# Kernel optimization log

Measured on AMD Instinct MI355X. Metric: run time of the kernel, lower is better.

The kernel has to match this reference:

```python
import jax, jax.numpy as jnp
import numpy as np

H, F, K, R = 8, 64, 10, 256  # num_heads, in_features, num_sines, num_realizations
B, L = 4, 2048


def setup_inputs() -> dict:
    key = jax.random.key(0)
    k1, k2, k3, k4, k5, k6 = jax.random.split(key, 6)
    return {
        "queries": jax.random.normal(k1, (B, L, H, F), dtype=jnp.float32),
        "keys": jax.random.normal(k2, (B, L, H, F), dtype=jnp.float32),
        "z": jax.random.normal(k3, (B, H, F, 2 * K, R), dtype=jnp.float32),
        "freqs": jax.random.normal(k4, (H, F, K), dtype=jnp.float32),
        "offsets": jax.random.normal(k5, (H, F, K), dtype=jnp.float32),
        "gains": jax.random.normal(k6, (H, F, K), dtype=jnp.float32),
    }


def reference(queries, keys, z, freqs, offsets, gains):
    h, f_dim, k_sines = freqs.shape
    length = queries.shape[1]
    r = z.shape[-1]
    # split positional / non-positional features (rest is empty here: key_dim == in_features)
    q_pos, q_rest = queries[..., :f_dim], queries[..., f_dim:]
    k_pos, k_rest = keys[..., :f_dim], keys[..., f_dim:]

    idx = jnp.arange(length, dtype=queries.dtype)  # linspace(0, L-1, L)
    fr = jax.nn.sigmoid(freqs)[:, :, None, :] / 2.0          # [H, F, 1, K]
    base = 2.0 * jnp.pi * fr * idx[None, None, :, None]       # [H, F, L, K]
    ph_q = base + offsets[:, :, None, :]
    ph_k = base
    # stack(cos, sin) on last axis then flatten -> interleaved cos0,sin0,... : [H, F, L, 2K]
    omega_q = jnp.stack([jnp.cos(ph_q), jnp.sin(ph_q)], axis=-1).reshape(h, f_dim, length, 2 * k_sines)
    omega_k = jnp.stack([jnp.cos(ph_k), jnp.sin(ph_k)], axis=-1).reshape(h, f_dim, length, 2 * k_sines)

    g = jnp.tile(jax.nn.softplus(gains), (1, 1, 2))           # [H, F, 2K] (block-repeated, as in torch .repeat)
    zs = z * g[None, :, :, :, None] / np.sqrt(r * f_dim).astype(np.float32)  # [B, H, F, 2K, R]

    # fused double contraction over f (in_features) and s (2K sines); equals
    # (omega @ z) permuted then multiplied by queries and summed over in_features
    qhat = jnp.einsum('hfls,bhfsr,blhf->blhr', omega_q, zs, q_pos)  # [B, L, H, R]
    khat = jnp.einsum('hfls,bhfsr,blhf->blhr', omega_k, zs, k_pos)

    qhat = jnp.concatenate([qhat, q_rest], axis=-1)
    khat = jnp.concatenate([khat, k_rest], axis=-1)
    return qhat, khat
```

## Files before the change

### kernel.cpp

```cpp
#include <hip/hip_runtime.h>
#include <math.h>


#define NH 8
#define NF 64
#define NK 10
#define NR 256
#define NB 4
#define NL 2048
#define KTOT 1280
#define BM 128
#define BK 32
#define NCH (KTOT/BK)
#define NFRAG_B 16
#define WS_NEEDED ((size_t)NB*NH*NCH*NFRAG_B*1024)

typedef __attribute__((ext_vector_type(8))) short short8;
typedef __attribute__((ext_vector_type(4))) float f32x4;
typedef __attribute__((ext_vector_type(4))) unsigned int u32x4;

static __device__ __forceinline__ unsigned short f2b(float f) {
    unsigned x = __float_as_uint(f);
    return (unsigned short)((x + 0x7FFFu + ((x >> 16) & 1u)) >> 16);
}
static __device__ __forceinline__ unsigned int pk2(float a, float b) {
    return (unsigned int)f2b(a) | ((unsigned int)f2b(b) << 16);
}
static __device__ __forceinline__ void gload_lds16(const void* g, void* l) {
    __builtin_amdgcn_global_load_lds(
        (const __attribute__((address_space(1))) unsigned int*)g,
        (__attribute__((address_space(3))) unsigned int*)l, 16, 0, 0);
}

__global__ __launch_bounds__(256)
void spe_prep(const float* __restrict__ z, const float* __restrict__ gains,
              unsigned char* __restrict__ bpack)
{
    __shared__ float s_g[NF*NK];
    const int ch  = blockIdx.x;
    const int bh  = blockIdx.y;
    const int h   = bh & 7;
    const int tid = threadIdx.x;
    for (int i = tid; i < NF*NK; i += 256)
        s_g[i] = log1pf(expf(gains[h*NF*NK + i])) * 0.0078125f;
    __syncthreads();
    const float* zb = z + (size_t)bh * KTOT * NR;
    unsigned char* dst = bpack + ((size_t)(bh*NCH + ch) * NFRAG_B) * 1024;
    #pragma unroll
    for (int it = 0; it < 4; ++it) {
        const int s  = tid + 256*it;
        const int fi = s >> 6;
        const int l  = s & 63;
        const int r  = fi*16 + (l & 15);
        const int k0 = ch*BK + (l >> 4)*8;
        u32x4 wv;
        #pragma unroll
        for (int jp = 0; jp < 4; ++jp) {
            const int ka = k0 + 2*jp, kb = ka + 1;
            const int fa = (ka*3277) >> 16; int sa = ka - fa*20; if (sa >= NK) sa -= NK;
            const int fb = (kb*3277) >> 16; int sb = kb - fb*20; if (sb >= NK) sb -= NK;
            const float va = zb[(size_t)ka*NR + r] * s_g[fa*NK + sa];
            const float vb = zb[(size_t)kb*NR + r] * s_g[fb*NK + sb];
            wv[jp] = pk2(va, vb);
        }
        *(u32x4*)(dst + (size_t)s*16) = wv;
    }
}

#define OFF_B0  0
#define OFF_B1  16384
#define OFF_A   32768
#define OFF_POS 40960
#define OFF_FR  57344
#define OFF_OF  59904
#define SMEM_SZ 62464

__global__ __launch_bounds__(512, 4)
void spe_main(const float* __restrict__ queries, const float* __restrict__ keys,
              const float* __restrict__ freqs, const float* __restrict__ offsets,
              const unsigned char* __restrict__ bpack, float* __restrict__ out)
{
    __shared__ __attribute__((aligned(16))) unsigned char smem[SMEM_SZ];
    const int tid  = threadIdx.x;
    const int lane = tid & 63;
    const int w    = tid >> 6;
    const int l0   = blockIdx.x * BM;
    const int bh   = blockIdx.y;
    const int b = bh >> 3, h = bh & 7;
    const int isK  = blockIdx.z;

    float* ld_fr = (float*)(smem + OFF_FR);
    float* ld_of = (float*)(smem + OFF_OF);
    unsigned short* pos_t = (unsigned short*)(smem + OFF_POS);

    for (int i = tid; i < NF*NK; i += 512) {
        const float fv = freqs[h*NF*NK + i];
        ld_fr[i] = 0.5f / (1.0f + expf(-fv));
        ld_of[i] = isK ? 0.0f : offsets[h*NF*NK + i] * 0.15915494309189535f;
    }
    {
        const float* pos = isK ? keys : queries;
        const int r  = tid >> 2;
        const int f0 = (tid & 3) * 16;
        const float* src = pos + ((size_t)((b*NL + l0 + r)*NH + h))*NF + f0;
        #pragma unroll
        for (int j = 0; j < 4; ++j) {
            const float4 v = *(const float4*)(src + j*4);
            const int f = f0 + j*4;
            pos_t[(f+0)*BM + r] = f2b(v.x);
            pos_t[(f+1)*BM + r] = f2b(v.y);
            pos_t[(f+2)*BM + r] = f2b(v.z);
            pos_t[(f+3)*BM + r] = f2b(v.w);
        }
    }
    __syncthreads();

    const unsigned char* bp = bpack + (size_t)bh * ((size_t)NCH*NFRAG_B*1024);
    const int fi0 = w*2;
    gload_lds16(bp + (size_t)fi0*1024 + lane*16,       smem + OFF_B0 + (fi0  <<10));
    gload_lds16(bp + (size_t)(fi0+1)*1024 + lane*16,   smem + OFF_B0 + ((fi0+1)<<10));

    const int wm = w >> 2, wn = w & 3;
    f32x4 acc[4][4];
    #pragma unroll
    for (int mi = 0; mi < 4; ++mi)
        #pragma unroll
        for (int ni = 0; ni < 4; ++ni)
            acc[mi][ni] = (f32x4){0.f, 0.f, 0.f, 0.f};

    const int a_oct  = w >> 1;
    const int a_m    = ((w & 1) << 6) | lane;
    const float lf   = (float)(l0 + a_m);
    const int a_byte = (((w & 1)*4 + (lane >> 4)) << 10) + (a_oct << 8) + ((lane & 15) << 4);

    auto synthA = [&](int t) -> u32x4 {
        u32x4 wv;
        #pragma unroll
        for (int jp = 0; jp < 4; ++jp) {
            const int kk   = t*BK + a_oct*8 + 2*jp;
            const int f    = (kk*3277) >> 16;
            const int srem = kk - f*20;
            const int kidx = f*NK + (srem >> 1);
            const float x  = __builtin_amdgcn_fractf(ld_of[kidx] + ld_fr[kidx]*lf);
            const float c  = __builtin_amdgcn_cosf(x);
            const float sn = __builtin_amdgcn_sinf(x);
            const float p  = __uint_as_float(((unsigned)pos_t[f*BM + a_m]) << 16);
            wv[jp] = pk2(c*p, sn*p);
        }
        return wv;
    };

    u32x4 wv = synthA(0);

    for (int t = 0; t < NCH; ++t) {
        unsigned char* Bcur = smem + ((t & 1) ? OFF_B1 : OFF_B0);
        unsigned char* Bnxt = smem + ((t & 1) ? OFF_B0 : OFF_B1);

        asm volatile("s_waitcnt vmcnt(0)" ::: "memory");
        __builtin_amdgcn_sched_barrier(0);
        __builtin_amdgcn_s_barrier();

        if (t + 1 < NCH) {
            gload_lds16(bp + (size_t)((t+1)*NFRAG_B + fi0)*1024 + lane*16,
                        Bnxt + (fi0<<10));
            gload_lds16(bp + (size_t)((t+1)*NFRAG_B + fi0+1)*1024 + lane*16,
                        Bnxt + ((fi0+1)<<10));
        }

        *(u32x4*)(smem + OFF_A + a_byte) = wv;
        asm volatile("s_waitcnt lgkmcnt(0)" ::: "memory");
        __builtin_amdgcn_sched_barrier(0);
        __builtin_amdgcn_s_barrier();

        short8 bf[4];
        #pragma unroll
        for (int ni = 0; ni < 4; ++ni)
            bf[ni] = *(const short8*)(Bcur + ((wn*4 + ni) << 10) + (lane << 4));

        if (t + 1 < NCH) wv = synthA(t + 1);

        #pragma unroll
        for (int mi = 0; mi < 4; ++mi) {
            const short8 af = *(const short8*)(smem + OFF_A + ((wm*4 + mi) << 10) + (lane << 4));
            #pragma unroll
            for (int ni = 0; ni < 4; ++ni)
                acc[mi][ni] = __builtin_amdgcn_mfma_f32_16x16x32_bf16(af, bf[ni], acc[mi][ni], 0, 0, 0);
        }
    }

    const size_t qk_off = (size_t)isK * ((size_t)NB*NL*NH*NR);
    const int row_l = (lane >> 4) * 4;
    const int col_r = lane & 15;
    #pragma unroll
    for (int mi = 0; mi < 4; ++mi) {
        const int lg = l0 + wm*64 + mi*16 + row_l;
        #pragma unroll
        for (int ni = 0; ni < 4; ++ni) {
            const int rg = wn*64 + ni*16 + col_r;
            const f32x4 v = acc[mi][ni];
            #pragma unroll
            for (int q = 0; q < 4; ++q)
                out[qk_off + ((size_t)((b*NL + lg + q)*NH + h))*NR + rg] = v[q];
        }
    }
}

#define FOFF_B   0
#define FOFF_A   32768
#define FOFF_POS 49152
#define FOFF_FR  65536
#define FOFF_OFS 68096
#define FOFF_GS  70656
#define FSMEM_SZ 73216

__global__ __launch_bounds__(512, 4)
void spe_mfma_fb(const float* __restrict__ queries, const float* __restrict__ keys,
                 const float* __restrict__ z, const float* __restrict__ freqs,
                 const float* __restrict__ offsets, const float* __restrict__ gains,
                 float* __restrict__ out)
{
    __shared__ __attribute__((aligned(16))) unsigned char smem[FSMEM_SZ];
    const int tid = threadIdx.x, lane = tid & 63;
    const int l0 = blockIdx.x * BM, bh = blockIdx.y;
    const int b = bh >> 3, h = bh & 7, isK = blockIdx.z;
    float* ld_fr = (float*)(smem + FOFF_FR);
    float* ld_of = (float*)(smem + FOFF_OFS);
    float* ld_gs = (float*)(smem + FOFF_GS);
    unsigned short* pos_t = (unsigned short*)(smem + FOFF_POS);
    for (int i = tid; i < NF*NK; i += 512) {
        const float fv = freqs[h*NF*NK + i];
        ld_fr[i] = 0.5f / (1.0f + expf(-fv));
        ld_of[i] = isK ? 0.0f : offsets[h*NF*NK + i] * 0.15915494309189535f;
        ld_gs[i] = log1pf(expf(gains[h*NF*NK + i])) * 0.0078125f;
    }
    {
        const float* pos = isK ? keys : queries;
        #pragma unroll
        for (int i = 0; i < 4; ++i) {
            const int lrow = (tid >> 4) + 32*i;
            const int f0 = (tid & 15) * 4;
            const float4 v = *(const float4*)(pos + ((size_t)((b*NL + l0 + lrow)*NH + h))*NF + f0);
            pos_t[(f0+0)*BM + lrow] = f2b(v.x); pos_t[(f0+1)*BM + lrow] = f2b(v.y);
            pos_t[(f0+2)*BM + lrow] = f2b(v.z); pos_t[(f0+3)*BM + lrow] = f2b(v.w);
        }
    }
    __syncthreads();
    const int w = tid >> 6, wm = w >> 2, wn = w & 3;
    f32x4 acc[4][4];
    #pragma unroll
    for (int mi = 0; mi < 4; ++mi)
        #pragma unroll
        for (int ni = 0; ni < 4; ++ni) acc[mi][ni] = (f32x4){0.f,0.f,0.f,0.f};
    const float* zbh = z + (size_t)(b*NH + h) * ((size_t)KTOT*NR);
    for (int ch = 0; ch < KTOT/64; ++ch) {
        const int fs0 = ch * 64;
        #pragma unroll
        for (int i = 0; i < 4; ++i) {
            const int tau = tid + 512*i, r = tau & 255, krun = tau >> 8;
            const float* zp = zbh + (size_t)(fs0 + krun*8)*NR + r;
            u32x4 wv2;
            #pragma unroll
            for (int jp = 0; jp < 4; ++jp) {
                const int fs = fs0 + krun*8 + 2*jp;
                const int f = (fs*3277) >> 16; const int rem = fs - f*20;
                const int km = (rem >= NK) ? rem - NK : rem;
                const int kn = ((rem+1) >= NK && (rem+1) < 2*NK) ? rem+1-NK : rem+1;
                const float sc0 = ld_gs[f*NK + km], sc1 = ld_gs[f*NK + (kn < NK ? kn : kn-NK)];
                wv2[jp] = pk2(zp[(2*jp)*NR]*sc0, zp[(2*jp+1)*NR]*sc1);
            }
            *(u32x4*)(smem + FOFF_B + ((((krun>>2)*16) + (r>>4)) << 10)
                                    + ((((krun&3)*16) + (r&15)) << 4)) = wv2;
        }
        #pragma unroll
        for (int i = 0; i < 2; ++i) {
            const int tau = tid + 512*i, m = tau & 127, krun = tau >> 7;
            const float lff = (float)(l0 + m);
            u32x4 wv2;
            #pragma unroll
            for (int jp = 0; jp < 4; ++jp) {
                const int fs = fs0 + krun*8 + 2*jp;
                const int f = (fs*3277) >> 16; const int rem = fs - f*20;
                const int kidx = f*NK + (rem >> 1);
                const float x = __builtin_amdgcn_fractf(ld_of[kidx] + ld_fr[kidx]*lff);
                const float c = __builtin_amdgcn_cosf(x), sn = __builtin_amdgcn_sinf(x);
                const float p = __uint_as_float(((unsigned)pos_t[f*BM + m]) << 16);
                wv2[jp] = pk2(c*p, sn*p);
            }
            *(u32x4*)(smem + FOFF_A + ((((krun>>2)*8) + (m>>4)) << 10)
                                    + ((((krun&3)*16) + (m&15)) << 4)) = wv2;
        }
        __syncthreads();
        #pragma unroll
        for (int ks = 0; ks < 2; ++ks) {
            short8 bf[4];
            #pragma unroll
            for (int ni = 0; ni < 4; ++ni)
                bf[ni] = *(const short8*)(smem + FOFF_B + ((ks*16 + wn*4 + ni) << 10) + (lane << 4));
            #pragma unroll
            for (int mi = 0; mi < 4; ++mi) {
                const short8 af = *(const short8*)(smem + FOFF_A + ((ks*8 + wm*4 + mi) << 10) + (lane << 4));
                #pragma unroll
                for (int ni = 0; ni < 4; ++ni)
                    acc[mi][ni] = __builtin_amdgcn_mfma_f32_16x16x32_bf16(af, bf[ni], acc[mi][ni], 0, 0, 0);
            }
        }
        __syncthreads();
    }
    const size_t qk_off = (size_t)isK * ((size_t)NB*NL*NH*NR);
    const int row_l = (lane >> 4) * 4, col_r = lane & 15;
    #pragma unroll
    for (int mi = 0; mi < 4; ++mi) {
        const int lg = l0 + wm*64 + mi*16 + row_l;
        #pragma unroll
        for (int ni = 0; ni < 4; ++ni) {
            const int rg = wn*64 + ni*16 + col_r;
            const f32x4 v = acc[mi][ni];
            #pragma unroll
            for (int q = 0; q < 4; ++q)
                out[qk_off + ((size_t)((b*NL + lg + q)*NH + h))*NR + rg] = v[q];
        }
    }
}

extern "C" void kernel_launch(void* const* d_in, const int* in_sizes, int n_in,
                              void* d_out, int out_size, void* d_ws, size_t ws_size,
                              hipStream_t stream) {
    const float* queries = (const float*)d_in[0];
    const float* keys    = (const float*)d_in[1];
    const float* z       = (const float*)d_in[2];
    const float* freqs   = (const float*)d_in[3];
    const float* offsets = (const float*)d_in[4];
    const float* gains   = (const float*)d_in[5];
    float* out = (float*)d_out;

    if (ws_size >= WS_NEEDED) {
        unsigned char* bpack = (unsigned char*)d_ws;
        spe_prep<<<dim3(NCH, NB*NH), 256, 0, stream>>>(z, gains, bpack);
        spe_main<<<dim3(NL/BM, NB*NH, 2), 512, 0, stream>>>(queries, keys, freqs, offsets, bpack, out);
    } else {
        spe_mfma_fb<<<dim3(NL/BM, NB*NH, 2), 512, 0, stream>>>(queries, keys, z, freqs, offsets, gains, out);
    }
}
```

Measured before the change: 133.6 us.

## Fuse query and key tiles per block, sharing sin/cos via angle-addition

Each block now handles 64 positions for both queries and keys instead of 128 positions for one of them. The query phase is derived from the key phase with the angle-addition identity and precomputed cos/sin of the offsets, so only one sin/cos pair is evaluated per element. The change also switches to a hardware packed bf16 convert and XOR-swizzles the A-tile LDS layout to reduce bank conflicts. The grid stays the same size, and z tiles are loaded once for both outputs, at the cost of slightly more LDS and a few extra multiplies.

```diff
diff --git a/kernel.cpp b/kernel.cpp
--- a/kernel.cpp
+++ b/kernel.cpp
@@ -18,6 +18,7 @@
 typedef __attribute__((ext_vector_type(8))) short short8;
 typedef __attribute__((ext_vector_type(4))) float f32x4;
 typedef __attribute__((ext_vector_type(4))) unsigned int u32x4;
+typedef __attribute__((ext_vector_type(2))) unsigned int u32x2;
 
 static __device__ __forceinline__ unsigned short f2b(float f) {
     unsigned x = __float_as_uint(f);
@@ -25,6 +26,11 @@
 }
 static __device__ __forceinline__ unsigned int pk2(float a, float b) {
     return (unsigned int)f2b(a) | ((unsigned int)f2b(b) << 16);
+}
+static __device__ __forceinline__ unsigned int cvtpk(float lo, float hi) {
+    unsigned int r;
+    asm("v_cvt_pk_bf16_f32 %0, %1, %2" : "=v"(r) : "v"(lo), "v"(hi));
+    return r;
 }
 static __device__ __forceinline__ void gload_lds16(const void* g, void* l) {
     __builtin_amdgcn_global_load_lds(
@@ -72,8 +78,9 @@
 #define OFF_A   32768
 #define OFF_POS 40960
 #define OFF_FR  57344
-#define OFF_OF  59904
-#define SMEM_SZ 62464
+#define OFF_CO  59904
+#define OFF_SO  62464
+#define SMEM_SZ 65024
 
 __global__ __launch_bounds__(512, 4)
 void spe_main(const float* __restrict__ queries, const float* __restrict__ keys,
@@ -84,33 +91,38 @@
     const int tid  = threadIdx.x;
     const int lane = tid & 63;
     const int w    = tid >> 6;
-    const int l0   = blockIdx.x * BM;
+    const int l0   = blockIdx.x * 64;
     const int bh   = blockIdx.y;
     const int b = bh >> 3, h = bh & 7;
-    const int isK  = blockIdx.z;
 
     float* ld_fr = (float*)(smem + OFF_FR);
-    float* ld_of = (float*)(smem + OFF_OF);
+    float* ld_co = (float*)(smem + OFF_CO);
+    float* ld_so = (float*)(smem + OFF_SO);
     unsigned short* pos_t = (unsigned short*)(smem + OFF_POS);
 
     for (int i = tid; i < NF*NK; i += 512) {
         const float fv = freqs[h*NF*NK + i];
         ld_fr[i] = 0.5f / (1.0f + expf(-fv));
-        ld_of[i] = isK ? 0.0f : offsets[h*NF*NK + i] * 0.15915494309189535f;
+        const float xo = __builtin_amdgcn_fractf(offsets[h*NF*NK + i] * 0.15915494309189535f);
+        ld_co[i] = __builtin_amdgcn_cosf(xo);
+        ld_so[i] = __builtin_amdgcn_sinf(xo);
     }
     {
-        const float* pos = isK ? keys : queries;
         const int r  = tid >> 2;
         const int f0 = (tid & 3) * 16;
-        const float* src = pos + ((size_t)((b*NL + l0 + r)*NH + h))*NF + f0;
+        const int rl = r & 63;
+        const float* src = (r < 64)
+            ? queries + ((size_t)((b*NL + l0 + rl)*NH + h))*NF + f0
+            : keys    + ((size_t)((b*NL + l0 + rl)*NH + h))*NF + f0;
+        unsigned short* pdst = pos_t + ((r >> 6) << 12);
         #pragma unroll
         for (int j = 0; j < 4; ++j) {
             const float4 v = *(const float4*)(src + j*4);
             const int f = f0 + j*4;
-            pos_t[(f+0)*BM + r] = f2b(v.x);
-            pos_t[(f+1)*BM + r] = f2b(v.y);
-            pos_t[(f+2)*BM + r] = f2b(v.z);
-            pos_t[(f+3)*BM + r] = f2b(v.w);
+            pdst[(f+0)*64 + rl] = f2b(v.x);
+            pdst[(f+1)*64 + rl] = f2b(v.y);
+            pdst[(f+2)*64 + rl] = f2b(v.z);
+            pdst[(f+3)*64 + rl] = f2b(v.w);
         }
     }
     __syncthreads();
@@ -128,29 +140,38 @@
         for (int ni = 0; ni < 4; ++ni)
             acc[mi][ni] = (f32x4){0.f, 0.f, 0.f, 0.f};
 
-    const int a_oct  = w >> 1;
-    const int a_m    = ((w & 1) << 6) | lane;
-    const float lf   = (float)(l0 + a_m);
-    const int a_byte = (((w & 1)*4 + (lane >> 4)) << 10) + (a_oct << 8) + ((lane & 15) << 4);
-
-    auto synthA = [&](int t) -> u32x4 {
-        u32x4 wv;
-        #pragma unroll
-        for (int jp = 0; jp < 4; ++jp) {
-            const int kk   = t*BK + a_oct*8 + 2*jp;
+    const int rq   = tid & 63;
+    const int oct  = (tid >> 6) & 3;
+    const int half = tid >> 8;
+    const float lf = (float)(l0 + rq);
+    const unsigned short* posq = pos_t;
+    const unsigned short* posk = pos_t + 4096;
+    const int a_log_q = ((rq >> 4) << 10) + ((oct*16 + (rq & 15)) << 4) + (half << 3);
+    const int aw_q = a_log_q ^ (((rq >> 4) & 3) << 5);
+    const int aw_k = (a_log_q + 4096) ^ (((rq >> 4) & 3) << 5);
+
+    auto synthA = [&](int t, u32x2& q01, u32x2& k01) {
+        #pragma unroll
+        for (int p = 0; p < 2; ++p) {
+            const int kk   = t*BK + oct*8 + (half*2 + p)*2;
             const int f    = (kk*3277) >> 16;
             const int srem = kk - f*20;
             const int kidx = f*NK + (srem >> 1);
-            const float x  = __builtin_amdgcn_fractf(ld_of[kidx] + ld_fr[kidx]*lf);
-            const float c  = __builtin_amdgcn_cosf(x);
-            const float sn = __builtin_amdgcn_sinf(x);
-            const float p  = __uint_as_float(((unsigned)pos_t[f*BM + a_m]) << 16);
-            wv[jp] = pk2(c*p, sn*p);
-        }
-        return wv;
+            const float x  = __builtin_amdgcn_fractf(ld_fr[kidx] * lf);
+            const float ck = __builtin_amdgcn_cosf(x);
+            const float sk = __builtin_amdgcn_sinf(x);
+            const float co = ld_co[kidx], so = ld_so[kidx];
+            const float cq = ck*co - sk*so;
+            const float sq = sk*co + ck*so;
+            const float pq = __uint_as_float(((unsigned)posq[f*64 + rq]) << 16);
+            const float pk = __uint_as_float(((unsigned)posk[f*64 + rq]) << 16);
+            q01[p] = cvtpk(cq*pq, sq*pq);
+            k01[p] = cvtpk(ck*pk, sk*pk);
+        }
     };
 
-    u32x4 wv = synthA(0);
+    u32x2 q01, k01;
+    synthA(0, q01, k01);
 
     for (int t = 0; t < NCH; ++t) {
         unsigned char* Bcur = smem + ((t & 1) ? OFF_B1 : OFF_B0);
@@ -167,7 +188,8 @@
                         Bnxt + ((fi0+1)<<10));
         }
 
-        *(u32x4*)(smem + OFF_A + a_byte) = wv;
+        *(u32x2*)(smem + OFF_A + aw_q) = q01;
+        *(u32x2*)(smem + OFF_A + aw_k) = k01;
         asm volatile("s_waitcnt lgkmcnt(0)" ::: "memory");
         __builtin_amdgcn_sched_barrier(0);
         __builtin_amdgcn_s_barrier();
@@ -177,23 +199,25 @@
         for (int ni = 0; ni < 4; ++ni)
             bf[ni] = *(const short8*)(Bcur + ((wn*4 + ni) << 10) + (lane << 4));
 
-        if (t + 1 < NCH) wv = synthA(t + 1);
+        if (t + 1 < NCH) synthA(t + 1, q01, k01);
 
         #pragma unroll
         for (int mi = 0; mi < 4; ++mi) {
-            const short8 af = *(const short8*)(smem + OFF_A + ((wm*4 + mi) << 10) + (lane << 4));
+            const int g    = wm*4 + mi;
+            const int aoff = (g << 10) + (lane << 4);
+            const short8 af = *(const short8*)(smem + OFF_A + (aoff ^ ((g & 3) << 5)));
             #pragma unroll
             for (int ni = 0; ni < 4; ++ni)
                 acc[mi][ni] = __builtin_amdgcn_mfma_f32_16x16x32_bf16(af, bf[ni], acc[mi][ni], 0, 0, 0);
         }
     }
 
-    const size_t qk_off = (size_t)isK * ((size_t)NB*NL*NH*NR);
+    const size_t qk_off = (size_t)wm * ((size_t)NB*NL*NH*NR);
     const int row_l = (lane >> 4) * 4;
     const int col_r = lane & 15;
     #pragma unroll
     for (int mi = 0; mi < 4; ++mi) {
-        const int lg = l0 + wm*64 + mi*16 + row_l;
+        const int lg = l0 + mi*16 + row_l;
         #pragma unroll
         for (int ni = 0; ni < 4; ++ni) {
             const int rg = wn*64 + ni*16 + col_r;
@@ -336,7 +360,7 @@
     if (ws_size >= WS_NEEDED) {
         unsigned char* bpack = (unsigned char*)d_ws;
         spe_prep<<<dim3(NCH, NB*NH), 256, 0, stream>>>(z, gains, bpack);
-        spe_main<<<dim3(NL/BM, NB*NH, 2), 512, 0, stream>>>(queries, keys, freqs, offsets, bpack, out);
+        spe_main<<<dim3(NL/64, NB*NH), 512, 0, stream>>>(queries, keys, freqs, offsets, bpack, out);
     } else {
         spe_mfma_fb<<<dim3(NL/BM, NB*NH, 2), 512, 0, stream>>>(queries, keys, z, freqs, offsets, gains, out);
     }
```

Measured after the change: 126.1 us. -5.7%, faster.
